# Performance work log

Hardware: AMD Instinct MI355X
Metric: run time of the kernel (lower is better)

Reference implementation:

```python
import jax, jax.numpy as jnp
import numpy as np
import math


def setup_inputs() -> dict:
    key = jax.random.key(0)
    ks = jax.random.split(key, 6)
    B, C, H, W = 4, 384, 64, 64
    nd = 12
    d = C // nd  # 32 = projected channel width
    return {
        "x": jax.random.normal(ks[0], (B, C, H, W), jnp.float32),
        "xe": jax.random.normal(ks[1], (B, C, H, W), jnp.float32),
        "Wq": jax.random.normal(ks[2], (d, C), jnp.float32) * 0.02,      # 1x1 conv C -> d, no bias
        "Wkv": jax.random.normal(ks[3], (2 * d, C), jnp.float32) * 0.02,  # 1x1 conv C -> 2d, no bias
        "Wout": jax.random.normal(ks[4], (C, d, 3, 3), jnp.float32) * 0.02,  # 3x3 conv d -> C
        "bout": jnp.zeros((C,), jnp.float32),
        "n_div": 12,
    }


def reference(x, xe, Wq, Wkv, Wout, bout, n_div):
    B, C, H, W = x.shape
    Y, X = xe.shape[-2], xe.shape[-1]
    n_head = 1
    hd = C // (n_head * n_div)  # head_dim
    # 1x1 conv projections as einsums
    q = jnp.einsum('dc,bchw->bdhw', Wq, x).reshape(B, n_head, hd, H, W)
    kv = jnp.einsum('dc,bchw->bdhw', Wkv, xe).reshape(B, n_head, 2 * hd, Y, X)
    k, v = kv[:, :, :hd], kv[:, :, hd:]
    # full pairwise spatial attention scores [B, n_head, H, W, Y, X]
    scale = 1.0 / math.sqrt(C // n_div)
    attn = jnp.einsum('bnchw,bncyx->bnhwyx', q, k) * scale
    attn = jax.nn.softmax(attn.reshape(B, n_head, H, W, Y * X), axis=-1)
    attn = attn.reshape(B, n_head, H, W, Y, X)
    out = jnp.einsum('bnhwyx,bncyx->bnchw', attn, v).reshape(B, C // n_div, H, W)
    # 3x3 conv with padding 1, plus bias, then residual
    out = jax.lax.conv_general_dilated(
        out, Wout, window_strides=(1, 1), padding='SAME',
        dimension_numbers=('NCHW', 'OIHW', 'NCHW'))
    out = out + bout[None, :, None, None]
    return out + x
```

## Files before the change

kernel.cpp:

```cpp
#include <hip/hip_runtime.h>
#include <hip/hip_bf16.h>
#include <math.h>

#define B_   4
#define C_   384
#define HD_  32
#define P_   4096
#define PADP 4356
#define QSC_ 0.2550889266f

typedef __attribute__((ext_vector_type(4))) float f32x4;
typedef __attribute__((ext_vector_type(8))) short short8;

static __device__ inline unsigned cvt_pk(float lo, float hi) {
    unsigned r;
    asm("v_cvt_pk_bf16_f32 %0, %1, %2" : "=v"(r) : "v"(lo), "v"(hi));
    return r;
}
static __device__ inline float exp2a(float x) {
    float r;
    asm("v_exp_f32 %0, %1" : "=v"(r) : "v"(x));
    return r;
}
static __device__ inline short bf16_bits(float a) {
    __hip_bfloat16 x = __float2bfloat16(a);
    return *reinterpret_cast<short*>(&x);
}

__global__ void repack_kernel(const float* __restrict__ Wq,
                              const float* __restrict__ Wkv,
                              const float* __restrict__ Wout,
                              short* __restrict__ Wball,
                              short* __restrict__ Wbc,
                              unsigned* __restrict__ aoT32) {
    int idx = blockIdx.x * 256 + threadIdx.x;
    if (idx < B_ * 260 * 16) {
        int j = idx & 15;
        int p = (idx >> 4) % 260;
        int b = idx / (260 * 16);
        int hh, ww;
        if (p < 66)       { hh = 0;  ww = p; }
        else if (p < 132) { hh = 65; ww = p - 66; }
        else { int i = p - 132; hh = 1 + (i >> 1); ww = (i & 1) * 65; }
        aoT32[((size_t)b * PADP + hh * 66 + ww) * 16 + j] = 0;
    }
    if (idx < 96 * C_) {
        int r = idx / C_, c = idx % C_;
        float v = (r < 32) ? Wq[r * C_ + c] * QSC_ : Wkv[(r - 32) * C_ + c];
        Wball[idx] = bf16_bits(v);
    }
    int j = idx - 96 * C_;
    if (j >= 0 && j < 9 * 384 * 32) {
        int ci = j & 31;
        int co = (j >> 5) % 384;
        int kk = j / (384 * 32);
        int ky = kk / 3, kx = kk % 3;
        Wbc[j] = bf16_bits(Wout[((co * 32 + ci) * 3 + ky) * 3 + kx]);
    }
}

__global__ __launch_bounds__(768)
void proj_kernel(const float* __restrict__ x, const float* __restrict__ xe,
                 const short* __restrict__ Wball,
                 short* __restrict__ qT, short* __restrict__ kT,
                 short* __restrict__ vT) {
    int b = blockIdx.y;
    int p0 = blockIdx.x << 5;
    int t = threadIdx.x, w = t >> 6, l = t & 63, lq = l & 15, h = l >> 4;
    int mt = w >> 1, pg = w & 1;
    int p = p0 + pg * 16 + lq;
    const float* in = (mt < 2) ? x : xe;
    const float* xb = in + (size_t)b * C_ * P_ + p;
    const short* Ap = Wball + (size_t)(mt * 16 + lq) * C_ + h * 8;
    f32x4 acc = {0.f, 0.f, 0.f, 0.f};
    for (int ks = 0; ks < 12; ++ks) {
        float xv[8];
        #pragma unroll
        for (int jj = 0; jj < 8; ++jj)
            xv[jj] = xb[(size_t)(ks * 32 + h * 8 + jj) * P_];
        unsigned u[4];
        #pragma unroll
        for (int jj = 0; jj < 4; ++jj) u[jj] = cvt_pk(xv[2 * jj], xv[2 * jj + 1]);
        short8 bf;
        __builtin_memcpy(&bf, u, 16);
        short8 af = *(const short8*)(Ap + ks * 32);
        acc = __builtin_amdgcn_mfma_f32_16x16x32_bf16(af, bf, acc, 0, 0, 0);
    }
    if (mt < 4) {
        short* dst = (mt < 2) ? qT : kT;
        int d = (mt & 1) * 16 + h * 4;
        uint2 u;
        u.x = cvt_pk(acc[0], acc[1]);
        u.y = cvt_pk(acc[2], acc[3]);
        *(uint2*)(dst + ((size_t)b * P_ + p) * HD_ + d) = u;
    } else {
        int d = (mt - 4) * 16 + h * 4;
        #pragma unroll
        for (int r = 0; r < 4; ++r)
            vT[((size_t)b * HD_ + d + r) * P_ + p] = bf16_bits(acc[r]);
    }
}

__global__ __launch_bounds__(512, 4)
void attn_mfma_kernel(const short* __restrict__ qT,
                      const short* __restrict__ kT,
                      const short* __restrict__ vT,
                      short* __restrict__ aoT) {
    __shared__ unsigned p_lds[8][1024];
    __shared__ float o_sh[32][33];
    __shared__ float l_sh[32];

    int blk = blockIdx.x;
    int b = blk >> 7;
    int q0 = (blk & 127) << 5;
    int t = threadIdx.x, w = t >> 6, l = t & 63, lq = l & 15, h = l >> 4;

    for (int i = t; i < 32 * 33; i += 512) ((float*)o_sh)[i] = 0.f;
    if (t < 32) l_sh[t] = 0.f;

    const short* qTb = qT + ((size_t)b * P_ + q0) * HD_;
    const short* kTb = kT + (size_t)b * P_ * HD_;
    const short* vb  = vT + (size_t)b * HD_ * P_;

    short8 qf0 = *(const short8*)(qTb + lq * HD_ + h * 8);
    short8 qf1 = *(const short8*)(qTb + (16 + lq) * HD_ + h * 8);

    f32x4 o00 = {0.f,0.f,0.f,0.f}, o01 = {0.f,0.f,0.f,0.f};
    f32x4 o10 = {0.f,0.f,0.f,0.f}, o11 = {0.f,0.f,0.f,0.f};
    float lsum0 = 0.f, lsum1 = 0.f;
    unsigned* myp = &p_lds[w][0];
    int swz = (lq & 7) << 4;

    int key_base = w * 512;
    short8 kf[4];
    {
        const short* kp = kTb + (size_t)(key_base + lq) * HD_ + h * 8;
        #pragma unroll
        for (int tt = 0; tt < 4; ++tt) kf[tt] = *(const short8*)(kp + tt * 16 * HD_);
    }
    __syncthreads();

    for (int kt = 0; kt < 8; ++kt) {
        int key0 = key_base + kt * 64;
        const short* vp = vb + (size_t)lq * P_ + key0 + h * 8;
        short8 vf0 = *(const short8*)(vp);
        short8 vf1 = *(const short8*)(vp + 32);
        short8 vf2 = *(const short8*)(vp + 16 * P_);
        short8 vf3 = *(const short8*)(vp + 16 * P_ + 32);

        f32x4 st0[4], st1[4];
        __builtin_amdgcn_s_setprio(1);
        #pragma unroll
        for (int tt = 0; tt < 4; ++tt) {
            st0[tt] = __builtin_amdgcn_mfma_f32_16x16x32_bf16(kf[tt], qf0,
                          (f32x4){0.f,0.f,0.f,0.f}, 0, 0, 0);
            st1[tt] = __builtin_amdgcn_mfma_f32_16x16x32_bf16(kf[tt], qf1,
                          (f32x4){0.f,0.f,0.f,0.f}, 0, 0, 0);
        }
        __builtin_amdgcn_s_setprio(0);

        if (kt < 7) {
            const short* kp = kTb + (size_t)(key0 + 64 + lq) * HD_ + h * 8;
            #pragma unroll
            for (int tt = 0; tt < 4; ++tt) kf[tt] = *(const short8*)(kp + tt * 16 * HD_);
        }

        #pragma unroll
        for (int qt = 0; qt < 2; ++qt) {
            f32x4* st = qt ? st1 : st0;
            float e[16];
            #pragma unroll
            for (int tt = 0; tt < 4; ++tt)
                #pragma unroll
                for (int r = 0; r < 4; ++r) e[tt * 4 + r] = exp2a(st[tt][r]);
            float ls = 0.f;
            #pragma unroll
            for (int i = 0; i < 16; i += 4)
                ls += (e[i] + e[i + 1]) + (e[i + 2] + e[i + 3]);
            if (qt) lsum1 += ls; else lsum0 += ls;
            unsigned* row = myp + ((qt * 16 + lq) * 128 >> 2);
            #pragma unroll
            for (int tt = 0; tt < 4; ++tt) {
                int u0 = tt * 32 + h * 8;
                row[((u0 + 0) ^ swz) >> 2] = cvt_pk(e[tt * 4 + 0], e[tt * 4 + 1]);
                row[((u0 + 4) ^ swz) >> 2] = cvt_pk(e[tt * 4 + 2], e[tt * 4 + 3]);
            }
        }

        short8 pb00, pb01, pb10, pb11;
        __builtin_memcpy(&pb00, (const char*)myp + lq * 128        + ((h * 16 + 0)  ^ swz), 16);
        __builtin_memcpy(&pb01, (const char*)myp + lq * 128        + ((h * 16 + 64) ^ swz), 16);
        __builtin_memcpy(&pb10, (const char*)myp + (16 + lq) * 128 + ((h * 16 + 0)  ^ swz), 16);
        __builtin_memcpy(&pb11, (const char*)myp + (16 + lq) * 128 + ((h * 16 + 64) ^ swz), 16);

        __builtin_amdgcn_s_setprio(1);
        o00 = __builtin_amdgcn_mfma_f32_16x16x32_bf16(vf0, pb00, o00, 0, 0, 0);
        o00 = __builtin_amdgcn_mfma_f32_16x16x32_bf16(vf1, pb01, o00, 0, 0, 0);
        o01 = __builtin_amdgcn_mfma_f32_16x16x32_bf16(vf0, pb10, o01, 0, 0, 0);
        o01 = __builtin_amdgcn_mfma_f32_16x16x32_bf16(vf1, pb11, o01, 0, 0, 0);
        o10 = __builtin_amdgcn_mfma_f32_16x16x32_bf16(vf2, pb00, o10, 0, 0, 0);
        o10 = __builtin_amdgcn_mfma_f32_16x16x32_bf16(vf3, pb01, o10, 0, 0, 0);
        o11 = __builtin_amdgcn_mfma_f32_16x16x32_bf16(vf2, pb10, o11, 0, 0, 0);
        o11 = __builtin_amdgcn_mfma_f32_16x16x32_bf16(vf3, pb11, o11, 0, 0, 0);
        __builtin_amdgcn_s_setprio(0);
    }

    lsum0 += __shfl_xor(lsum0, 16); lsum0 += __shfl_xor(lsum0, 32);
    lsum1 += __shfl_xor(lsum1, 16); lsum1 += __shfl_xor(lsum1, 32);

    #pragma unroll
    for (int r = 0; r < 4; ++r) {
        atomicAdd(&o_sh[h * 4 + r][lq],           o00[r]);
        atomicAdd(&o_sh[h * 4 + r][16 + lq],      o01[r]);
        atomicAdd(&o_sh[16 + h * 4 + r][lq],      o10[r]);
        atomicAdd(&o_sh[16 + h * 4 + r][16 + lq], o11[r]);
    }
    if (h == 0) {
        atomicAdd(&l_sh[lq],      lsum0);
        atomicAdd(&l_sh[16 + lq], lsum1);
    }
    __syncthreads();

    {
        int qq = t >> 4;
        int d0 = (t & 15) * 2;
        float inv = 1.f / l_sh[qq];
        float v0 = o_sh[d0][qq], v1 = o_sh[d0 + 1][qq];
        int p = q0 + qq;
        int hh = p >> 6, ww2 = p & 63;
        unsigned* dst = (unsigned*)(aoT +
            ((size_t)b * PADP + (hh + 1) * 66 + (ww2 + 1)) * HD_ + d0);
        *dst = cvt_pk(v0 * inv, v1 * inv);
    }
}

__global__ __launch_bounds__(512)
void conv_mfma_kernel(const short* __restrict__ Wbc,
                      const short* __restrict__ aoT,
                      const float* __restrict__ bout,
                      const float* __restrict__ x,
                      float* __restrict__ out) {
    int blk = blockIdx.x;
    int b = blk >> 7;
    int p0 = (blk & 127) << 5;
    int t = threadIdx.x;
    int w = t >> 6, l = t & 63, lq = l & 15, h = l >> 4;
    int co0 = w * 48;

    const short* aob = aoT + (size_t)b * PADP * HD_;
    const short* bptr[2];
    #pragma unroll
    for (int n = 0; n < 2; ++n) {
        int p = p0 + n * 16 + lq;
        int hh = p >> 6, ww = p & 63;
        bptr[n] = aob + (size_t)(hh * 66 + ww) * HD_ + h * 8;
    }
    const short* aptr = Wbc + (size_t)(co0 + lq) * 32 + h * 8;

    f32x4 acc[3][2];
    #pragma unroll
    for (int m = 0; m < 3; ++m)
        #pragma unroll
        for (int n = 0; n < 2; ++n) acc[m][n] = (f32x4){0.f, 0.f, 0.f, 0.f};

    short8 Bf0 = *(const short8*)(bptr[0]);
    short8 Bf1 = *(const short8*)(bptr[1]);
    #pragma unroll
    for (int kk = 0; kk < 9; ++kk) {
        short8 nB0, nB1;
        if (kk < 8) {
            int ky = (kk + 1) / 3, kx = (kk + 1) % 3;
            nB0 = *(const short8*)(bptr[0] + (ky * 66 + kx) * HD_);
            nB1 = *(const short8*)(bptr[1] + (ky * 66 + kx) * HD_);
        } else { nB0 = Bf0; nB1 = Bf1; }
        #pragma unroll
        for (int m = 0; m < 3; ++m) {
            short8 Af = *(const short8*)(aptr + kk * 12288 + m * 512);
            acc[m][0] = __builtin_amdgcn_mfma_f32_16x16x32_bf16(Af, Bf0, acc[m][0], 0, 0, 0);
            acc[m][1] = __builtin_amdgcn_mfma_f32_16x16x32_bf16(Af, Bf1, acc[m][1], 0, 0, 0);
        }
        Bf0 = nB0; Bf1 = nB1;
    }

    #pragma unroll
    for (int m = 0; m < 3; ++m) {
        #pragma unroll
        for (int r = 0; r < 4; ++r) {
            int co = co0 + m * 16 + h * 4 + r;
            float bias = bout[co];
            #pragma unroll
            for (int n = 0; n < 2; ++n) {
                int p = p0 + n * 16 + lq;
                size_t idx = ((size_t)b * C_ + co) * P_ + p;
                out[idx] = acc[m][n][r] + bias + x[idx];
            }
        }
    }
}

extern "C" void kernel_launch(void* const* d_in, const int* in_sizes, int n_in,
                              void* d_out, int out_size, void* d_ws, size_t ws_size,
                              hipStream_t stream) {
    const float* x    = (const float*)d_in[0];
    const float* xe   = (const float*)d_in[1];
    const float* Wq   = (const float*)d_in[2];
    const float* Wkv  = (const float*)d_in[3];
    const float* Wout = (const float*)d_in[4];
    const float* bout = (const float*)d_in[5];
    float* out = (float*)d_out;

    short* qT    = (short*)d_ws;
    short* kT    = qT  + (size_t)B_ * P_ * HD_;
    short* vT    = kT  + (size_t)B_ * P_ * HD_;
    short* aoT   = vT  + (size_t)B_ * P_ * HD_;
    short* Wball = aoT + (size_t)B_ * PADP * HD_;
    short* Wbc   = Wball + 96 * C_;

    repack_kernel<<<576, 256, 0, stream>>>(Wq, Wkv, Wout, Wball, Wbc, (unsigned*)aoT);
    proj_kernel<<<dim3(128, B_), 768, 0, stream>>>(x, xe, Wball, qT, kT, vT);
    attn_mfma_kernel<<<B_ * 128, 512, 0, stream>>>(qT, kT, vT, aoT);
    conv_mfma_kernel<<<B_ * 128, 512, 0, stream>>>(Wbc, aoT, bout, x, out);
}
```

Measured before the change: 90.49 us.

## Store V in key-chunked blocked layout and prefetch V fragments one tile ahead

The projection kernel now writes V into a blocked layout of 32-key chunks by 32 channels. Each attention wave's V fragment loads therefore touch contiguous 1-2KB regions instead of rows strided by P. The attention loop also software-pipelines the V loads, issuing the next tile's fragments before the softmax and PV MFMAs of the current tile. This is meant to cut global load latency and the cost of strided access, at the price of extra registers (four more short8 values live) that could hurt occupancy under launch_bounds(512,4).

```diff
diff --git a/kernel.cpp b/kernel.cpp
--- a/kernel.cpp
+++ b/kernel.cpp
@@ -63,7 +63,7 @@
 void proj_kernel(const float* __restrict__ x, const float* __restrict__ xe,
                  const short* __restrict__ Wball,
                  short* __restrict__ qT, short* __restrict__ kT,
-                 short* __restrict__ vT) {
+                 short* __restrict__ vC) {
     int b = blockIdx.y;
     int p0 = blockIdx.x << 5;
     int t = threadIdx.x, w = t >> 6, l = t & 63, lq = l & 15, h = l >> 4;
@@ -94,17 +94,18 @@
         u.y = cvt_pk(acc[2], acc[3]);
         *(uint2*)(dst + ((size_t)b * P_ + p) * HD_ + d) = u;
     } else {
-        int d = (mt - 4) * 16 + h * 4;
+        int dt = mt - 4;
+        size_t base = (((size_t)b * 128 + (p >> 5)) * 32 + dt * 16 + h * 4) * 32 + (p & 31);
         #pragma unroll
         for (int r = 0; r < 4; ++r)
-            vT[((size_t)b * HD_ + d + r) * P_ + p] = bf16_bits(acc[r]);
+            vC[base + (size_t)r * 32] = bf16_bits(acc[r]);
     }
 }
 
 __global__ __launch_bounds__(512, 4)
 void attn_mfma_kernel(const short* __restrict__ qT,
                       const short* __restrict__ kT,
-                      const short* __restrict__ vT,
+                      const short* __restrict__ vC,
                       short* __restrict__ aoT) {
     __shared__ unsigned p_lds[8][1024];
     __shared__ float o_sh[32][33];
@@ -120,7 +121,7 @@
 
     const short* qTb = qT + ((size_t)b * P_ + q0) * HD_;
     const short* kTb = kT + (size_t)b * P_ * HD_;
-    const short* vb  = vT + (size_t)b * HD_ * P_;
+    const short* vCb = vC + (size_t)b * 131072;
 
     short8 qf0 = *(const short8*)(qTb + lq * HD_ + h * 8);
     short8 qf1 = *(const short8*)(qTb + (16 + lq) * HD_ + h * 8);
@@ -138,15 +139,18 @@
         #pragma unroll
         for (int tt = 0; tt < 4; ++tt) kf[tt] = *(const short8*)(kp + tt * 16 * HD_);
     }
+    short8 vf0, vf1, vf2, vf3;
+    {
+        const short* vp = vCb + ((size_t)(key_base >> 5) * 32 + lq) * 32 + h * 8;
+        vf0 = *(const short8*)(vp);
+        vf1 = *(const short8*)(vp + 1024);
+        vf2 = *(const short8*)(vp + 512);
+        vf3 = *(const short8*)(vp + 1536);
+    }
     __syncthreads();
 
     for (int kt = 0; kt < 8; ++kt) {
         int key0 = key_base + kt * 64;
-        const short* vp = vb + (size_t)lq * P_ + key0 + h * 8;
-        short8 vf0 = *(const short8*)(vp);
-        short8 vf1 = *(const short8*)(vp + 32);
-        short8 vf2 = *(const short8*)(vp + 16 * P_);
-        short8 vf3 = *(const short8*)(vp + 16 * P_ + 32);
 
         f32x4 st0[4], st1[4];
         __builtin_amdgcn_s_setprio(1);
@@ -163,6 +167,15 @@
             const short* kp = kTb + (size_t)(key0 + 64 + lq) * HD_ + h * 8;
             #pragma unroll
             for (int tt = 0; tt < 4; ++tt) kf[tt] = *(const short8*)(kp + tt * 16 * HD_);
+        }
+        short8 nv0, nv1, nv2, nv3;
+        {
+            int nkey = key0 + (kt < 7 ? 64 : 0);
+            const short* vp = vCb + ((size_t)(nkey >> 5) * 32 + lq) * 32 + h * 8;
+            nv0 = *(const short8*)(vp);
+            nv1 = *(const short8*)(vp + 1024);
+            nv2 = *(const short8*)(vp + 512);
+            nv3 = *(const short8*)(vp + 1536);
         }
 
         #pragma unroll
@@ -203,6 +216,8 @@
         o11 = __builtin_amdgcn_mfma_f32_16x16x32_bf16(vf2, pb10, o11, 0, 0, 0);
         o11 = __builtin_amdgcn_mfma_f32_16x16x32_bf16(vf3, pb11, o11, 0, 0, 0);
         __builtin_amdgcn_s_setprio(0);
+
+        vf0 = nv0; vf1 = nv1; vf2 = nv2; vf3 = nv3;
     }
 
     lsum0 += __shfl_xor(lsum0, 16); lsum0 += __shfl_xor(lsum0, 32);
@@ -311,13 +326,13 @@
 
     short* qT    = (short*)d_ws;
     short* kT    = qT  + (size_t)B_ * P_ * HD_;
-    short* vT    = kT  + (size_t)B_ * P_ * HD_;
-    short* aoT   = vT  + (size_t)B_ * P_ * HD_;
+    short* vC    = kT  + (size_t)B_ * P_ * HD_;
+    short* aoT   = vC  + (size_t)B_ * 131072;
     short* Wball = aoT + (size_t)B_ * PADP * HD_;
     short* Wbc   = Wball + 96 * C_;
 
     repack_kernel<<<576, 256, 0, stream>>>(Wq, Wkv, Wout, Wball, Wbc, (unsigned*)aoT);
-    proj_kernel<<<dim3(128, B_), 768, 0, stream>>>(x, xe, Wball, qT, kT, vT);
-    attn_mfma_kernel<<<B_ * 128, 512, 0, stream>>>(qT, kT, vT, aoT);
+    proj_kernel<<<dim3(128, B_), 768, 0, stream>>>(x, xe, Wball, qT, kT, vC);
+    attn_mfma_kernel<<<B_ * 128, 512, 0, stream>>>(qT, kT, vC, aoT);
     conv_mfma_kernel<<<B_ * 128, 512, 0, stream>>>(Wbc, aoT, bout, x, out);
 }
```

Measured after the change: 96.94 us. 7.1% more time.

## Split attention key range across two blocks and combine partials in a normalize kernel

Applied to the files above, without the earlier changes.

The attention grid doubles from 512 to 1024 blocks, and each block processes half of the key range (2048 keys, 256 per warp). Each block writes unnormalized fp32 partial outputs and row sums to workspace. A new norm kernel then adds the two halves, divides by the summed denominator, converts to bf16 and writes into the padded conv input. The goal is to fill the GPU better and give more blocks per CU to hide latency. The cost is the per-block fixed overhead (loading Q, zeroing LDS, LDS atomic reduction) paid twice as often, fp32 partial traffic, and one extra kernel launch.

```diff
diff --git a/kernel.cpp b/kernel.cpp
--- a/kernel.cpp
+++ b/kernel.cpp
@@ -105,14 +105,16 @@
 void attn_mfma_kernel(const short* __restrict__ qT,
                       const short* __restrict__ kT,
                       const short* __restrict__ vT,
-                      short* __restrict__ aoT) {
+                      float* __restrict__ aoF, float* __restrict__ lF) {
     __shared__ unsigned p_lds[8][1024];
     __shared__ float o_sh[32][33];
     __shared__ float l_sh[32];
 
     int blk = blockIdx.x;
-    int b = blk >> 7;
-    int q0 = (blk & 127) << 5;
+    int b = blk >> 8;
+    int rem = blk & 255;
+    int half = rem >> 7;
+    int q0 = (rem & 127) << 5;
     int t = threadIdx.x, w = t >> 6, l = t & 63, lq = l & 15, h = l >> 4;
 
     for (int i = t; i < 32 * 33; i += 512) ((float*)o_sh)[i] = 0.f;
@@ -131,7 +133,7 @@
     unsigned* myp = &p_lds[w][0];
     int swz = (lq & 7) << 4;
 
-    int key_base = w * 512;
+    int key_base = half * 2048 + w * 256;
     short8 kf[4];
     {
         const short* kp = kTb + (size_t)(key_base + lq) * HD_ + h * 8;
@@ -140,7 +142,7 @@
     }
     __syncthreads();
 
-    for (int kt = 0; kt < 8; ++kt) {
+    for (int kt = 0; kt < 4; ++kt) {
         int key0 = key_base + kt * 64;
         const short* vp = vb + (size_t)lq * P_ + key0 + h * 8;
         short8 vf0 = *(const short8*)(vp);
@@ -159,7 +161,7 @@
         }
         __builtin_amdgcn_s_setprio(0);
 
-        if (kt < 7) {
+        if (kt < 3) {
             const short* kp = kTb + (size_t)(key0 + 64 + lq) * HD_ + h * 8;
             #pragma unroll
             for (int tt = 0; tt < 4; ++tt) kf[tt] = *(const short8*)(kp + tt * 16 * HD_);
@@ -224,14 +226,37 @@
     {
         int qq = t >> 4;
         int d0 = (t & 15) * 2;
-        float inv = 1.f / l_sh[qq];
-        float v0 = o_sh[d0][qq], v1 = o_sh[d0 + 1][qq];
-        int p = q0 + qq;
-        int hh = p >> 6, ww2 = p & 63;
-        unsigned* dst = (unsigned*)(aoT +
-            ((size_t)b * PADP + (hh + 1) * 66 + (ww2 + 1)) * HD_ + d0);
-        *dst = cvt_pk(v0 * inv, v1 * inv);
-    }
+        float* dst = aoF + (size_t)half * B_ * P_ * HD_
+                   + ((size_t)b * P_ + q0 + qq) * HD_ + d0;
+        dst[0] = o_sh[d0][qq];
+        dst[1] = o_sh[d0 + 1][qq];
+    }
+    if (t < 32)
+        lF[(size_t)half * B_ * P_ + (size_t)b * P_ + q0 + t] = l_sh[t];
+}
+
+__global__ __launch_bounds__(256)
+void norm_kernel(const float* __restrict__ aoF, const float* __restrict__ lF,
+                 short* __restrict__ aoT) {
+    int pid = blockIdx.x * 256 + threadIdx.x;
+    int b = pid >> 12, p = pid & (P_ - 1);
+    const float* a0 = aoF + ((size_t)b * P_ + p) * HD_;
+    const float* a1 = a0 + (size_t)B_ * P_ * HD_;
+    float ltot = lF[(size_t)b * P_ + p] + lF[(size_t)B_ * P_ + (size_t)b * P_ + p];
+    float inv = 1.f / ltot;
+    unsigned u[16];
+    #pragma unroll
+    for (int j = 0; j < 8; ++j) {
+        f32x4 s0 = *(const f32x4*)(a0 + j * 4);
+        f32x4 s1 = *(const f32x4*)(a1 + j * 4);
+        f32x4 s = s0 + s1;
+        u[2 * j]     = cvt_pk(s[0] * inv, s[1] * inv);
+        u[2 * j + 1] = cvt_pk(s[2] * inv, s[3] * inv);
+    }
+    int hh = p >> 6, ww = p & 63;
+    unsigned* dst = (unsigned*)(aoT + ((size_t)b * PADP + (hh + 1) * 66 + (ww + 1)) * HD_);
+    #pragma unroll
+    for (int j = 0; j < 16; ++j) dst[j] = u[j];
 }
 
 __global__ __launch_bounds__(512)
@@ -313,11 +338,14 @@
     short* kT    = qT  + (size_t)B_ * P_ * HD_;
     short* vT    = kT  + (size_t)B_ * P_ * HD_;
     short* aoT   = vT  + (size_t)B_ * P_ * HD_;
-    short* Wball = aoT + (size_t)B_ * PADP * HD_;
+    float* aoF   = (float*)(aoT + (size_t)B_ * PADP * HD_);
+    float* lF    = aoF + (size_t)2 * B_ * P_ * HD_;
+    short* Wball = (short*)(lF + (size_t)2 * B_ * P_);
     short* Wbc   = Wball + 96 * C_;
 
     repack_kernel<<<576, 256, 0, stream>>>(Wq, Wkv, Wout, Wball, Wbc, (unsigned*)aoT);
     proj_kernel<<<dim3(128, B_), 768, 0, stream>>>(x, xe, Wball, qT, kT, vT);
-    attn_mfma_kernel<<<B_ * 128, 512, 0, stream>>>(qT, kT, vT, aoT);
+    attn_mfma_kernel<<<B_ * 256, 512, 0, stream>>>(qT, kT, vT, aoF, lF);
+    norm_kernel<<<64, 256, 0, stream>>>(aoF, lF, aoT);
     conv_mfma_kernel<<<B_ * 128, 512, 0, stream>>>(Wbc, aoT, bout, x, out);
 }
```

Result: slower. 117.8 us (+30.2%).
